# Kernel tuning notes

Hardware: AMD Instinct MI355X
Metric: run time of the kernel (lower is better)

The kernel has to match this reference:

```python
import jax, jax.numpy as jnp
import numpy as np

P = 2        # patch size (all 3 dims)
NB = 8       # num_bands
N = 16       # d_state
DTR = 8      # dt_rank = d_model // 16
DCONV = 4    # d_conv
SMAX = 2.0   # smax_dt = smax_B = smax_C


def _ln(x, g, b):
    mu = x.mean(-1, keepdims=True)
    v = ((x - mu) ** 2).mean(-1, keepdims=True)
    return (x - mu) / jnp.sqrt(v + 1e-5) * g + b


def _silu(x):
    return x * jax.nn.sigmoid(x)


def _ssm_layer(x, band, m, rho, Win, bin_, convw, convb, Wx, Wdt, bdt, Alog, Dp,
               Wout, bout, edt, eB, eC, wr, wm):
    # x: [B, L, d_model] -> bidirectional conditioned selective scan (BiFCSSM)
    Bsz, L, _ = x.shape
    ED = convw.shape[0]
    xz = x @ Win + bin_
    xp, z = xz[..., :ED], xz[..., ED:]
    # depthwise causal conv1d over L
    xpad = jnp.pad(xp, ((0, 0), (DCONV - 1, 0), (0, 0)))
    xc = sum(xpad[:, k:k + L, :] * convw[:, k] for k in range(DCONV)) + convb
    xc = _silu(xc)
    dbl = xc @ Wx                                    # [B,L,DTR+2N]
    dt = jax.nn.softplus(dbl[..., :DTR] @ Wdt + bdt)  # [B,L,ED]
    # band/radius/mask conditioned modulation of delta, B, C
    s_dt = SMAX * jax.nn.sigmoid(edt[band][None] + wr[0] * rho[None] + wm[0] * m)
    s_B = SMAX * jax.nn.sigmoid(eB[band][None] + wr[1] * rho[None] + wm[1] * m)
    s_C = SMAX * jax.nn.sigmoid(eC[band][None] + wr[2] * rho[None] + wm[2] * m)
    dt = dt * s_dt[..., None]
    Bm = dbl[..., DTR:DTR + N] * s_B[..., None]       # [B,L,N]
    Cm = dbl[..., DTR + N:] * s_C[..., None]          # [B,L,N]
    A = -jnp.exp(Alog)                                # [ED,N]
    dA = jnp.exp(dt[..., None] * A)                   # [B,L,ED,N]
    dBu = (dA - 1.0) / A * Bm[:, :, None, :] * xc[..., None]   # exact ZOH
    dA_s = jnp.moveaxis(dA, 1, 0)
    dBu_s = jnp.moveaxis(dBu, 1, 0)
    C_s = jnp.moveaxis(Cm, 1, 0)
    h0 = jnp.zeros((Bsz, ED, N), x.dtype)

    def step(h, inp):
        a, bu, c = inp
        h = a * h + bu
        return h, jnp.einsum('ben,bn->be', h, c)

    _, yf = jax.lax.scan(step, h0, (dA_s, dBu_s, C_s))
    _, yb = jax.lax.scan(step, h0, (dA_s, dBu_s, C_s), reverse=True)
    y = jnp.moveaxis(yf + yb, 0, 1) + Dp * xc
    y = y * _silu(z)
    return y @ Wout + bout


def _fwd(kspace_ri, mask, pe_w, pe_b, pu_w, pu_b, ln_g, ln_b, fn_g, fn_b,
         cond_band, cond_rad_w, cond_mask_w, l0_Win, l0_bin, l0_convw, l0_convb,
         l0_Wx, l0_Wdt, l0_bdt, l0_Alog, l0_D, l0_Wout, l0_bout, l0_edt, l0_eB,
         l0_eC, l0_wr, l0_wm):
    Bsz, C, nx, ny, nz = kspace_ri.shape
    gx, gy, gz = nx // P, ny // P, nz // P
    L = gx * gy * gz
    # patch embed (Conv3d, kernel==stride) as blocked einsum
    xr = kspace_ri.reshape(Bsz, C, gx, P, gy, P, gz, P)
    x = jnp.einsum('bcxiyjzk,dcijk->bdxyz', xr, pe_w) + pe_b[None, :, None, None, None]
    DM = x.shape[1]
    x = x.reshape(Bsz, DM, L).transpose(0, 2, 1)               # [B,L,D]
    m = mask.reshape(Bsz, 1, gx, P, gy, P, gz, P).mean(axis=(3, 5, 7)).reshape(Bsz, L)
    m = jnp.clip(m, 0.0, 1.0)
    # raster scan ordering: identity permutation, rho_bar, band ids
    rho = jnp.arange(L, dtype=x.dtype) / float(L - 1)
    band = jnp.clip(jnp.floor(rho * NB).astype(jnp.int32), 0, NB - 1)
    # condition tokens
    cond = cond_band[band][None] + rho[None, :, None] * cond_rad_w + m[:, :, None] * cond_mask_w
    h = _ln(x + cond, ln_g, ln_b)
    h = h + _ssm_layer(_ln(h, fn_g, fn_b), band, m, rho, l0_Win, l0_bin, l0_convw,
                       l0_convb, l0_Wx, l0_Wdt, l0_bdt, l0_Alog, l0_D, l0_Wout,
                       l0_bout, l0_edt, l0_eB, l0_eC, l0_wr, l0_wm)
    # patch unembed (ConvTranspose3d, kernel==stride) as blocked einsum
    hg = h.transpose(0, 2, 1).reshape(Bsz, DM, gx, gy, gz)
    out = jnp.einsum('bdxyz,dcijk->bcxiyjzk', hg, pu_w).reshape(Bsz, C, nx, ny, nz)
    out = out + pu_b[None, :, None, None, None]
    return kspace_ri + out


def setup_inputs() -> dict:
    key = jax.random.key(0)
    ks = jax.random.split(key, 24)
    ED, DM, CIN = 256, 128, 16

    def nrm(k, shape, s):
        return jax.random.normal(k, shape, jnp.float32) * s

    return {
        'kspace_ri': jax.random.normal(ks[0], (1, CIN, 64, 64, 16), jnp.float32),
        'mask': jax.random.uniform(ks[1], (1, 1, 64, 64, 16), jnp.float32),
        'pe_w': nrm(ks[2], (DM, CIN, P, P, P), 0.09),
        'pe_b': nrm(ks[3], (DM,), 0.02),
        'pu_w': nrm(ks[4], (DM, CIN, P, P, P), 0.05),
        'pu_b': jnp.zeros((CIN,), jnp.float32),
        'ln_g': jnp.ones((DM,), jnp.float32),
        'ln_b': jnp.zeros((DM,), jnp.float32),
        'fn_g': jnp.ones((DM,), jnp.float32),
        'fn_b': jnp.zeros((DM,), jnp.float32),
        'cond_band': nrm(ks[5], (NB, DM), 0.02),
        'cond_rad_w': nrm(ks[6], (DM,), 0.02),
        'cond_mask_w': nrm(ks[7], (DM,), 0.02),
        'l0_Win': nrm(ks[8], (DM, 2 * ED), 0.05),
        'l0_bin': jnp.zeros((2 * ED,), jnp.float32),
        'l0_convw': nrm(ks[9], (ED, DCONV), 0.2),
        'l0_convb': jnp.zeros((ED,), jnp.float32),
        'l0_Wx': nrm(ks[10], (ED, DTR + 2 * N), 0.05),
        'l0_Wdt': nrm(ks[11], (DTR, ED), 0.1),
        'l0_bdt': jnp.full((ED,), -3.0, jnp.float32),
        'l0_Alog': jnp.log(jnp.tile(jnp.arange(1, N + 1, dtype=jnp.float32), (ED, 1))),
        'l0_D': jnp.ones((ED,), jnp.float32),
        'l0_Wout': nrm(ks[12], (ED, DM), 0.05),
        'l0_bout': jnp.zeros((DM,), jnp.float32),
        'l0_edt': nrm(ks[13], (NB,), 0.1),
        'l0_eB': nrm(ks[14], (NB,), 0.1),
        'l0_eC': nrm(ks[15], (NB,), 0.1),
        'l0_wr': nrm(ks[16], (3,), 0.1),
        'l0_wm': nrm(ks[17], (3,), 0.1),
    }


def reference(kspace_ri, mask, pe_w, pe_b, pu_w, pu_b, ln_g, ln_b, fn_g, fn_b,
              cond_band, cond_rad_w, cond_mask_w, l0_Win, l0_bin, l0_convw,
              l0_convb, l0_Wx, l0_Wdt, l0_bdt, l0_Alog, l0_D, l0_Wout, l0_bout,
              l0_edt, l0_eB, l0_eC, l0_wr, l0_wm):
    return _fwd(kspace_ri, mask, pe_w, pe_b, pu_w, pu_b, ln_g, ln_b, fn_g, fn_b,
                cond_band, cond_rad_w, cond_mask_w, l0_Win, l0_bin, l0_convw,
                l0_convb, l0_Wx, l0_Wdt, l0_bdt, l0_Alog, l0_D, l0_Wout, l0_bout,
                l0_edt, l0_eB, l0_eC, l0_wr, l0_wm)
```

## Files before the change

kernel.cpp:

```cpp
#include <hip/hip_runtime.h>
#include <hip/hip_bf16.h>

#define L_TOK 8192
#define NCh 256
#define CLh 32
#define LOG2E 1.44269504088896f

typedef short bf16x8 __attribute__((ext_vector_type(8)));
typedef float f32x4 __attribute__((ext_vector_type(4)));

static __device__ __forceinline__ float nexp2(float x) {
#if __has_builtin(__builtin_amdgcn_exp2f)
    return __builtin_amdgcn_exp2f(x);
#else
    return exp2f(x);
#endif
}
static __device__ __forceinline__ float sigm(float x) {
    return 1.f / (1.f + nexp2(-x * LOG2E));
}
static __device__ __forceinline__ ushort f2bf(float x) {
    union { float f; uint u; } v; v.f = x;
    uint r = v.u + 0x7fffu + ((v.u >> 16) & 1u);
    return (ushort)(r >> 16);
}
static __device__ __forceinline__ float bf2f(ushort h) {
    union { float f; uint u; } v; v.u = ((uint)h) << 16;
    return v.f;
}
static __device__ __forceinline__ void f2hl(float x, ushort* hi, ushort* lo) {
    ushort h = f2bf(x);
    *hi = h;
    *lo = f2bf(x - bf2f(h));
}

#define W_PE   0
#define W_WIN  16384
#define W_WOUT 81920
#define W_PU   114688
#define W_PROJ 131072
#define W_TOT  212992

__global__ __launch_bounds__(256) void prep_k(const float* __restrict__ pe_w, const float* __restrict__ Win,
                                              const float* __restrict__ Wx, const float* __restrict__ Wdt,
                                              const float* __restrict__ Wout, const float* __restrict__ pu_w,
                                              const float* __restrict__ mask,
                                              ushort* __restrict__ wH, ushort* __restrict__ wL,
                                              float* __restrict__ mbuf) {
    int b = blockIdx.x;
    if (b >= 832) {
        int l = (b - 832) * 256 + threadIdx.x;
        int xg = l >> 8, yg = (l >> 3) & 31, zg = l & 7;
        float s = 0.f;
        for (int i2 = 0; i2 < 2; ++i2)
            for (int j2 = 0; j2 < 2; ++j2)
                for (int k2 = 0; k2 < 2; ++k2)
                    s += mask[(2 * xg + i2) * 1024 + (2 * yg + j2) * 16 + 2 * zg + k2];
        s *= 0.125f;
        mbuf[l] = fminf(fmaxf(s, 0.f), 1.f);
        return;
    }
    int i = b * 256 + threadIdx.x;
    float v;
    if (i < 16384) {
        v = pe_w[i];
    } else if (i < 81920) {
        int j = i - 16384; int n = j >> 7, k = j & 127;
        v = Win[k * 512 + n];
    } else if (i < 114688) {
        int j = i - 81920; int n = j >> 8, k = j & 255;
        v = Wout[k * 128 + n];
    } else if (i < 131072) {
        int j = i - 114688; int n = j >> 7, k = j & 127;
        v = pu_w[k * 128 + n];
    } else {
        int j = i - 131072; int n = j >> 8, k = j & 255;
        if (n < 256) {
            float s = 0.f;
#pragma unroll
            for (int r = 0; r < 8; ++r) s += Wx[k * 40 + r] * Wdt[r * 256 + n];
            v = s;
        } else if (n < 288) {
            v = Wx[k * 40 + 8 + (n - 256)];
        } else {
            v = 0.f;
        }
    }
    ushort h, lo; f2hl(v, &h, &lo);
    wH[i] = h; wL[i] = lo;
}

__global__ __launch_bounds__(256) void embed_ln_k(const float* __restrict__ ks,
                                                  const ushort* __restrict__ wH, const ushort* __restrict__ wL,
                                                  const float* __restrict__ pe_b, const float* __restrict__ cond_band,
                                                  const float* __restrict__ cond_rad, const float* __restrict__ cond_mask,
                                                  const float* __restrict__ mbuf,
                                                  const float* __restrict__ ln_g, const float* __restrict__ ln_b,
                                                  const float* __restrict__ fn_g, const float* __restrict__ fn_b,
                                                  float* __restrict__ h_,
                                                  ushort* __restrict__ hnH, ushort* __restrict__ hnL) {
    __shared__ __align__(16) char smem[41472];
    ushort (*AsH)[72] = (ushort(*)[72])(smem);
    ushort (*AsL)[72] = (ushort(*)[72])(smem + 2304);
    ushort (*BsH)[72] = (ushort(*)[72])(smem + 4608);
    ushort (*BsL)[72] = (ushort(*)[72])(smem + 23040);
    float  (*Cs)[132] = (float(*)[132])(smem);

    const int tid = threadIdx.x;
    const int lane = tid & 63, wn = tid >> 6;
    const int ln = lane & 15, q = lane >> 4;
    const int mb = blockIdx.x * 16;

    f32x4 acc[2];
    acc[0] = (f32x4){0.f, 0.f, 0.f, 0.f};
    acc[1] = (f32x4){0.f, 0.f, 0.f, 0.f};

    for (int kc = 0; kc < 128; kc += 64) {
        __syncthreads();
        for (int u = tid; u < 1024; u += 256) {
            int r = u >> 6, kk = u & 63;
            int l = mb + r, k = kc + kk;
            int cc = k >> 3, ijk = k & 7;
            int xg = l >> 8, yg = (l >> 3) & 31, zg = l & 7;
            int i2 = (ijk >> 2) & 1, j2 = (ijk >> 1) & 1, k2 = ijk & 1;
            float v = ks[cc * 65536 + (2 * xg + i2) * 1024 + (2 * yg + j2) * 16 + 2 * zg + k2];
            ushort h, lo; f2hl(v, &h, &lo);
            AsH[r][kk] = h; AsL[r][kk] = lo;
        }
        for (int u = tid; u < 1024; u += 256) {
            int n = u >> 3, g = u & 7;
            *(uint4*)&BsH[n][g * 8] = *(const uint4*)&wH[W_PE + n * 128 + kc + g * 8];
            *(uint4*)&BsL[n][g * 8] = *(const uint4*)&wL[W_PE + n * 128 + kc + g * 8];
        }
        __syncthreads();
#pragma unroll
        for (int ks_ = 0; ks_ < 64; ks_ += 32) {
            const int kk = ks_ + q * 8;
            bf16x8 ah = *(const bf16x8*)&AsH[ln][kk];
            bf16x8 al = *(const bf16x8*)&AsL[ln][kk];
#pragma unroll
            for (int cb = 0; cb < 2; ++cb) {
                bf16x8 bh = *(const bf16x8*)&BsH[wn * 32 + cb * 16 + ln][kk];
                bf16x8 bl = *(const bf16x8*)&BsL[wn * 32 + cb * 16 + ln][kk];
                acc[cb] = __builtin_amdgcn_mfma_f32_16x16x32_bf16(ah, bh, acc[cb], 0, 0, 0);
                acc[cb] = __builtin_amdgcn_mfma_f32_16x16x32_bf16(ah, bl, acc[cb], 0, 0, 0);
                acc[cb] = __builtin_amdgcn_mfma_f32_16x16x32_bf16(al, bh, acc[cb], 0, 0, 0);
            }
        }
    }
    __syncthreads();
#pragma unroll
    for (int cb = 0; cb < 2; ++cb) {
#pragma unroll
        for (int r = 0; r < 4; ++r) {
            int row = q * 4 + r;
            int col = wn * 32 + cb * 16 + ln;
            int l = mb + row;
            float rho = (float)l * (1.0f / 8191.0f);
            int band = min(7, (int)(rho * 8.0f));
            Cs[row][col] = acc[cb][r] + pe_b[col] + cond_band[band * 128 + col]
                           + rho * cond_rad[col] + mbuf[l] * cond_mask[col];
        }
    }
    __syncthreads();
    {
        int row = tid >> 4, j = tid & 15;
        int l = mb + row;
        float v8[8];
        float s = 0.f, s2 = 0.f;
#pragma unroll
        for (int i = 0; i < 8; ++i) {
            float v = Cs[row][j * 8 + i];
            v8[i] = v; s += v; s2 += v * v;
        }
#pragma unroll
        for (int o = 1; o < 16; o <<= 1) { s += __shfl_xor(s, o, 16); s2 += __shfl_xor(s2, o, 16); }
        float mu = s * (1.f / 128.f);
        float var = s2 * (1.f / 128.f) - mu * mu;
        float rstd = rsqrtf(fmaxf(var, 0.f) + 1e-5f);
        float hv[8];
        s = 0.f; s2 = 0.f;
#pragma unroll
        for (int i = 0; i < 8; ++i) {
            int col = j * 8 + i;
            float h = (v8[i] - mu) * rstd * ln_g[col] + ln_b[col];
            hv[i] = h; s += h; s2 += h * h;
        }
#pragma unroll
        for (int i = 0; i < 8; i += 4)
            *(float4*)&h_[(size_t)l * 128 + j * 8 + i] = make_float4(hv[i], hv[i + 1], hv[i + 2], hv[i + 3]);
#pragma unroll
        for (int o = 1; o < 16; o <<= 1) { s += __shfl_xor(s, o, 16); s2 += __shfl_xor(s2, o, 16); }
        mu = s * (1.f / 128.f);
        var = s2 * (1.f / 128.f) - mu * mu;
        rstd = rsqrtf(fmaxf(var, 0.f) + 1e-5f);
        union { ushort u[8]; uint4 v4; } oh, ol;
#pragma unroll
        for (int i = 0; i < 8; ++i) {
            int col = j * 8 + i;
            float o2 = (hv[i] - mu) * rstd * fn_g[col] + fn_b[col];
            ushort hh, ll; f2hl(o2, &hh, &ll);
            oh.u[i] = hh; ol.u[i] = ll;
        }
        *(uint4*)&hnH[(size_t)l * 128 + j * 8] = oh.v4;
        *(uint4*)&hnL[(size_t)l * 128 + j * 8] = ol.v4;
    }
}

__global__ __launch_bounds__(256) void win_k(const ushort* __restrict__ Ah, const ushort* __restrict__ Al,
                                             const ushort* __restrict__ wH, const ushort* __restrict__ wL,
                                             const float* __restrict__ bin_,
                                             float* __restrict__ xp, float* __restrict__ sz) {
    __shared__ ushort AsH[64][72], AsL[64][72];
    __shared__ ushort BsH[64][72], BsL[64][72];
    const int tid = threadIdx.x;
    const int lane = tid & 63, wave = tid >> 6;
    const int wm = wave & 1, wn = wave >> 1;
    const int ln = lane & 15, q = lane >> 4;
    const int mb = blockIdx.x * 64, nb = blockIdx.y * 64;

    f32x4 acc[2][2];
#pragma unroll
    for (int rb = 0; rb < 2; ++rb)
#pragma unroll
        for (int cb = 0; cb < 2; ++cb) acc[rb][cb] = (f32x4){0.f, 0.f, 0.f, 0.f};

    for (int kc = 0; kc < 128; kc += 64) {
        __syncthreads();
        for (int u = tid; u < 512; u += 256) {
            int r = u >> 3, g = u & 7;
            size_t go = (size_t)(mb + r) * 128 + kc + g * 8;
            *(uint4*)&AsH[r][g * 8] = *(const uint4*)&Ah[go];
            *(uint4*)&AsL[r][g * 8] = *(const uint4*)&Al[go];
        }
        for (int u = tid; u < 512; u += 256) {
            int n = u >> 3, g = u & 7;
            size_t go = (size_t)(W_WIN) + (size_t)(nb + n) * 128 + kc + g * 8;
            *(uint4*)&BsH[n][g * 8] = *(const uint4*)&wH[go];
            *(uint4*)&BsL[n][g * 8] = *(const uint4*)&wL[go];
        }
        __syncthreads();
#pragma unroll
        for (int ks_ = 0; ks_ < 64; ks_ += 32) {
            const int kk = ks_ + q * 8;
            bf16x8 ah[2], al[2], bh[2], bl[2];
#pragma unroll
            for (int rb = 0; rb < 2; ++rb) {
                ah[rb] = *(const bf16x8*)&AsH[wm * 32 + rb * 16 + ln][kk];
                al[rb] = *(const bf16x8*)&AsL[wm * 32 + rb * 16 + ln][kk];
            }
#pragma unroll
            for (int cb = 0; cb < 2; ++cb) {
                bh[cb] = *(const bf16x8*)&BsH[wn * 32 + cb * 16 + ln][kk];
                bl[cb] = *(const bf16x8*)&BsL[wn * 32 + cb * 16 + ln][kk];
            }
#pragma unroll
            for (int rb = 0; rb < 2; ++rb)
#pragma unroll
                for (int cb = 0; cb < 2; ++cb) {
                    acc[rb][cb] = __builtin_amdgcn_mfma_f32_16x16x32_bf16(ah[rb], bh[cb], acc[rb][cb], 0, 0, 0);
                    acc[rb][cb] = __builtin_amdgcn_mfma_f32_16x16x32_bf16(ah[rb], bl[cb], acc[rb][cb], 0, 0, 0);
                    acc[rb][cb] = __builtin_amdgcn_mfma_f32_16x16x32_bf16(al[rb], bh[cb], acc[rb][cb], 0, 0, 0);
                }
        }
    }
#pragma unroll
    for (int rb = 0; rb < 2; ++rb)
#pragma unroll
        for (int cb = 0; cb < 2; ++cb)
#pragma unroll
            for (int r = 0; r < 4; ++r) {
                int l = mb + wm * 32 + rb * 16 + q * 4 + r;
                int col = nb + wn * 32 + cb * 16 + ln;
                float v = acc[rb][cb][r] + bin_[col];
                if (col < 256) {
                    xp[(size_t)l * 256 + col] = v;
                } else {
                    sz[(size_t)l * 256 + (col - 256)] = v * sigm(v);
                }
            }
}

__global__ __launch_bounds__(256) void conv_k(const float* __restrict__ xp, const float* __restrict__ convw,
                                              const float* __restrict__ convb, float* __restrict__ xc) {
    int id = blockIdx.x * 256 + threadIdx.x;
    int l = id >> 6, e4 = (id & 63) * 4;
    float4 cw[4];
#pragma unroll
    for (int j = 0; j < 4; ++j) cw[j] = *(const float4*)&convw[(e4 + j) * 4];
    float4 cb = *(const float4*)&convb[e4];
    float o[4] = {cb.x, cb.y, cb.z, cb.w};
#pragma unroll
    for (int k = 0; k < 4; ++k) {
        int lp = l - 3 + k;
        if (lp >= 0) {
            float4 t = *(const float4*)&xp[(size_t)lp * 256 + e4];
            o[0] += t.x * ((const float*)&cw[0])[k];
            o[1] += t.y * ((const float*)&cw[1])[k];
            o[2] += t.z * ((const float*)&cw[2])[k];
            o[3] += t.w * ((const float*)&cw[3])[k];
        }
    }
    float4 r;
    r.x = o[0] * sigm(o[0]);
    r.y = o[1] * sigm(o[1]);
    r.z = o[2] * sigm(o[2]);
    r.w = o[3] * sigm(o[3]);
    *(float4*)&xc[(size_t)l * 256 + e4] = r;
}

__global__ __launch_bounds__(256) void proj_k(const float* __restrict__ xc,
                                              const ushort* __restrict__ wH, const ushort* __restrict__ wL,
                                              const float* __restrict__ bdt, const float* __restrict__ mbuf,
                                              const float* __restrict__ edt, const float* __restrict__ eB,
                                              const float* __restrict__ eC, const float* __restrict__ wr,
                                              const float* __restrict__ wm,
                                              float* __restrict__ dt, float* __restrict__ Bm, float* __restrict__ Cm) {
    __shared__ ushort AsH[64][72], AsL[64][72];
    __shared__ ushort BsH[64][72], BsL[64][72];
    const int tid = threadIdx.x;
    const int lane = tid & 63, wave = tid >> 6;
    const int wm_ = wave & 1, wn = wave >> 1;
    const int ln = lane & 15, q = lane >> 4;
    const int mb = blockIdx.x * 64, nb = blockIdx.y * 64;

    f32x4 acc[2][2];
#pragma unroll
    for (int rb = 0; rb < 2; ++rb)
#pragma unroll
        for (int cb = 0; cb < 2; ++cb) acc[rb][cb] = (f32x4){0.f, 0.f, 0.f, 0.f};

    for (int kc = 0; kc < 256; kc += 64) {
        __syncthreads();
        for (int u = tid; u < 1024; u += 256) {
            int r = u >> 4, kq = u & 15;
            float4 v = *(const float4*)&xc[(size_t)(mb + r) * 256 + kc + kq * 4];
            union { ushort u[4]; uint2 v2; } hh, ll;
            f2hl(v.x, &hh.u[0], &ll.u[0]); f2hl(v.y, &hh.u[1], &ll.u[1]);
            f2hl(v.z, &hh.u[2], &ll.u[2]); f2hl(v.w, &hh.u[3], &ll.u[3]);
            *(uint2*)&AsH[r][kq * 4] = hh.v2;
            *(uint2*)&AsL[r][kq * 4] = ll.v2;
        }
        for (int u = tid; u < 512; u += 256) {
            int n = u >> 3, g = u & 7;
            size_t go = (size_t)(W_PROJ) + (size_t)(nb + n) * 256 + kc + g * 8;
            *(uint4*)&BsH[n][g * 8] = *(const uint4*)&wH[go];
            *(uint4*)&BsL[n][g * 8] = *(const uint4*)&wL[go];
        }
        __syncthreads();
#pragma unroll
        for (int ks_ = 0; ks_ < 64; ks_ += 32) {
            const int kk = ks_ + q * 8;
            bf16x8 ah[2], al[2], bh[2], bl[2];
#pragma unroll
            for (int rb = 0; rb < 2; ++rb) {
                ah[rb] = *(const bf16x8*)&AsH[wm_ * 32 + rb * 16 + ln][kk];
                al[rb] = *(const bf16x8*)&AsL[wm_ * 32 + rb * 16 + ln][kk];
            }
#pragma unroll
            for (int cb = 0; cb < 2; ++cb) {
                bh[cb] = *(const bf16x8*)&BsH[wn * 32 + cb * 16 + ln][kk];
                bl[cb] = *(const bf16x8*)&BsL[wn * 32 + cb * 16 + ln][kk];
            }
#pragma unroll
            for (int rb = 0; rb < 2; ++rb)
#pragma unroll
                for (int cb = 0; cb < 2; ++cb) {
                    acc[rb][cb] = __builtin_amdgcn_mfma_f32_16x16x32_bf16(ah[rb], bh[cb], acc[rb][cb], 0, 0, 0);
                    acc[rb][cb] = __builtin_amdgcn_mfma_f32_16x16x32_bf16(ah[rb], bl[cb], acc[rb][cb], 0, 0, 0);
                    acc[rb][cb] = __builtin_amdgcn_mfma_f32_16x16x32_bf16(al[rb], bh[cb], acc[rb][cb], 0, 0, 0);
                }
        }
    }
#pragma unroll
    for (int rb = 0; rb < 2; ++rb)
#pragma unroll
        for (int cb = 0; cb < 2; ++cb)
#pragma unroll
            for (int r = 0; r < 4; ++r) {
                int l = mb + wm_ * 32 + rb * 16 + q * 4 + r;
                int col = nb + wn * 32 + cb * 16 + ln;
                float v = acc[rb][cb][r];
                float rho = (float)l * (1.0f / 8191.0f);
                int band = min(7, (int)(rho * 8.0f));
                float mv = mbuf[l];
                if (col < 256) {
                    float sc0 = 2.0f * sigm(edt[band] + wr[0] * rho + wm[0] * mv);
                    float v2 = v + bdt[col];
                    float sp = (v2 > 20.f) ? v2 : log1pf(expf(v2));
                    dt[(size_t)l * 256 + col] = sp * sc0;
                } else if (col < 272) {
                    float sc1 = 2.0f * sigm(eB[band] + wr[1] * rho + wm[1] * mv);
                    Bm[(size_t)l * 16 + (col - 256)] = v * sc1;
                } else if (col < 288) {
                    float sc2 = 2.0f * sigm(eC[band] + wr[2] * rho + wm[2] * mv);
                    Cm[(size_t)l * 16 + (col - 272)] = v * sc2;
                }
            }
}

__global__ __launch_bounds__(256) void scan0_k(const float* __restrict__ dt, const float* __restrict__ xc,
                                               const float* __restrict__ Bm, const float* __restrict__ Alog,
                                               float* __restrict__ Hb, float* __restrict__ sdtb) {
    const int c = blockIdx.x, dir = blockIdx.y, e = threadIdx.x;
    __shared__ float bms[CLh][16];
    for (int idx = e; idx < CLh * 16; idx += 256)
        bms[idx >> 4][idx & 15] = Bm[c * (CLh * 16) + idx];
    float A2[16], iv[16], h[16];
#pragma unroll
    for (int n = 0; n < 16; ++n) {
        float ea = nexp2(Alog[e * 16 + n] * LOG2E);
        A2[n] = -ea * LOG2E;
        iv[n] = -1.0f / ea;
        h[n] = 0.f;
    }
    const int base = c * CLh;
    float cu[8], cx[8], nu[8], nx[8];
#pragma unroll
    for (int j = 0; j < 8; ++j) {
        int p = dir ? (CLh - 1 - j) : j;
        cu[j] = dt[(size_t)(base + p) * 256 + e];
        cx[j] = xc[(size_t)(base + p) * 256 + e];
    }
    __syncthreads();
    float sdt = 0.f;
#pragma unroll
    for (int g = 0; g < CLh / 8; ++g) {
        if (g + 1 < CLh / 8) {
#pragma unroll
            for (int j = 0; j < 8; ++j) {
                int s = (g + 1) * 8 + j;
                int p = dir ? (CLh - 1 - s) : s;
                nu[j] = dt[(size_t)(base + p) * 256 + e];
                nx[j] = xc[(size_t)(base + p) * 256 + e];
            }
        }
#pragma unroll
        for (int j = 0; j < 8; ++j) {
            int s = g * 8 + j;
            int p = dir ? (CLh - 1 - s) : s;
            float u = cu[j], xv = cx[j];
            union { float4 v[4]; float f[16]; } bb;
            const float4* bp = (const float4*)&bms[p][0];
            bb.v[0] = bp[0]; bb.v[1] = bp[1]; bb.v[2] = bp[2]; bb.v[3] = bp[3];
#pragma unroll
            for (int n = 0; n < 16; ++n) {
                float a = nexp2(A2[n] * u);
                float w = xv * bb.f[n] * iv[n];
                h[n] = a * (h[n] + w) - w;
            }
            sdt += u;
        }
#pragma unroll
        for (int j = 0; j < 8; ++j) { cu[j] = nu[j]; cx[j] = nx[j]; }
    }
    const size_t hofs = (size_t)(dir * NCh + c) * 4096 + e * 16;
#pragma unroll
    for (int j = 0; j < 4; ++j)
        *(float4*)&Hb[hofs + 4 * j] = make_float4(h[4 * j], h[4 * j + 1], h[4 * j + 2], h[4 * j + 3]);
    if (dir == 0) sdtb[c * 256 + e] = sdt;
}

__global__ __launch_bounds__(64) void combine_k(const float* __restrict__ Hb, float* __restrict__ Hpre,
                                                const float* __restrict__ sdtb, const float* __restrict__ Alog) {
    int id = blockIdx.x * 64 + threadIdx.x;
    int dir = id >> 12, en = id & 4095, e = en >> 4;
    float A2 = -nexp2(Alog[en] * LOG2E) * LOG2E;
    float hi = 0.f;
    for (int g = 0; g < NCh / 8; ++g) {
        float Pv[8], qv[8];
#pragma unroll
        for (int j = 0; j < 8; ++j) {
            int c = dir ? (NCh - 1 - (g * 8 + j)) : (g * 8 + j);
            Pv[j] = sdtb[c * 256 + e];
            qv[j] = Hb[(size_t)(dir * NCh + c) * 4096 + en];
        }
#pragma unroll
        for (int j = 0; j < 8; ++j) {
            int c = dir ? (NCh - 1 - (g * 8 + j)) : (g * 8 + j);
            float P = nexp2(A2 * Pv[j]);
            Hpre[(size_t)(dir * NCh + c) * 4096 + en] = hi;
            hi = P * hi + qv[j];
        }
    }
}

template <int DIR>
static __device__ __forceinline__ void scan_dir(const float* __restrict__ dt, const float* __restrict__ xc,
                                                int base, int e,
                                                const float (*bms)[16], const float (*cms)[16],
                                                const float* A2, const float* iv,
                                                float* h, float* yreg) {
    float cu[8], cx[8], nu[8], nx[8];
#pragma unroll
    for (int j = 0; j < 8; ++j) {
        const int p = DIR ? (CLh - 1 - j) : j;
        cu[j] = dt[(size_t)(base + p) * 256 + e];
        cx[j] = xc[(size_t)(base + p) * 256 + e];
    }
#pragma unroll
    for (int g = 0; g < CLh / 8; ++g) {
        if (g + 1 < CLh / 8) {
#pragma unroll
            for (int j = 0; j < 8; ++j) {
                const int s = (g + 1) * 8 + j;
                const int p = DIR ? (CLh - 1 - s) : s;
                nu[j] = dt[(size_t)(base + p) * 256 + e];
                nx[j] = xc[(size_t)(base + p) * 256 + e];
            }
        }
#pragma unroll
        for (int j = 0; j < 8; ++j) {
            const int s = g * 8 + j;
            const int p = DIR ? (CLh - 1 - s) : s;
            float u = cu[j], xv = cx[j];
            union { float4 v[4]; float f[16]; } bb, cc;
            const float4* bp = (const float4*)&bms[p][0];
            bb.v[0] = bp[0]; bb.v[1] = bp[1]; bb.v[2] = bp[2]; bb.v[3] = bp[3];
            const float4* cp = (const float4*)&cms[p][0];
            cc.v[0] = cp[0]; cc.v[1] = cp[1]; cc.v[2] = cp[2]; cc.v[3] = cp[3];
            float y = 0.f;
#pragma unroll
            for (int n = 0; n < 16; ++n) {
                float a = nexp2(A2[n] * u);
                float w = xv * bb.f[n] * iv[n];
                h[n] = a * (h[n] + w) - w;
                y += h[n] * cc.f[n];
            }
            yreg[p] = y;
        }
#pragma unroll
        for (int j = 0; j < 8; ++j) { cu[j] = nu[j]; cx[j] = nx[j]; }
    }
}

__global__ __launch_bounds__(512) void scan1g_k(const float* __restrict__ dt, const float* __restrict__ xc,
                                                const float* __restrict__ Bm, const float* __restrict__ Cm,
                                                const float* __restrict__ Alog, const float* __restrict__ Hpre,
                                                const float* __restrict__ sz, const float* __restrict__ Dp,
                                                ushort* __restrict__ AHo, ushort* __restrict__ ALo) {
    const int c = blockIdx.x;
    const int tid = threadIdx.x;
    const int dir = tid >> 8;
    const int e = tid & 255;
    __shared__ float bms[CLh][16];
    __shared__ float cms[CLh][16];
    __shared__ float ysum[CLh][256];
    for (int idx = tid; idx < CLh * 16; idx += 512) {
        bms[idx >> 4][idx & 15] = Bm[c * (CLh * 16) + idx];
        cms[idx >> 4][idx & 15] = Cm[c * (CLh * 16) + idx];
    }
    float A2[16], iv[16], h[16];
#pragma unroll
    for (int n = 0; n < 16; ++n) {
        float ea = nexp2(Alog[e * 16 + n] * LOG2E);
        A2[n] = -ea * LOG2E;
        iv[n] = -1.0f / ea;
    }
    const size_t hofs = (size_t)(dir * NCh + c) * 4096 + e * 16;
#pragma unroll
    for (int j = 0; j < 4; ++j) {
        float4 hv = *(const float4*)&Hpre[hofs + 4 * j];
        h[4 * j] = hv.x; h[4 * j + 1] = hv.y; h[4 * j + 2] = hv.z; h[4 * j + 3] = hv.w;
    }
    const int base = c * CLh;
    float yreg[CLh];
    __syncthreads();
    if (dir == 0) {
        scan_dir<0>(dt, xc, base, e, bms, cms, A2, iv, h, yreg);
    } else {
        scan_dir<1>(dt, xc, base, e, bms, cms, A2, iv, h, yreg);
    }
    __syncthreads();
    if (dir == 0) {
#pragma unroll
        for (int l = 0; l < CLh; ++l) ysum[l][e] = yreg[l];
    }
    __syncthreads();
    if (dir == 1) {
        float dpv = Dp[e];
#pragma unroll
        for (int l = 0; l < CLh; ++l) {
            size_t gl = (size_t)(base + l) * 256 + e;
            float a = (ysum[l][e] + yreg[l] + dpv * xc[gl]) * sz[gl];
            ushort hh, ll; f2hl(a, &hh, &ll);
            AHo[gl] = hh; ALo[gl] = ll;
        }
    }
}

__global__ __launch_bounds__(256) void wout_k(const ushort* __restrict__ AH, const ushort* __restrict__ AL,
                                              const ushort* __restrict__ wH, const ushort* __restrict__ wL,
                                              const float* __restrict__ bout, const float* __restrict__ h_,
                                              ushort* __restrict__ hfH, ushort* __restrict__ hfL) {
    __shared__ ushort AsH[32][72], AsL[32][72];
    __shared__ ushort BsH[64][72], BsL[64][72];
    const int tid = threadIdx.x;
    const int lane = tid & 63, wave = tid >> 6;
    const int wm = wave & 1, wn = wave >> 1;
    const int ln = lane & 15, q = lane >> 4;
    const int mb = blockIdx.x * 32, nb = blockIdx.y * 64;

    f32x4 acc[2];
    acc[0] = (f32x4){0.f, 0.f, 0.f, 0.f};
    acc[1] = (f32x4){0.f, 0.f, 0.f, 0.f};

    for (int kc = 0; kc < 256; kc += 64) {
        __syncthreads();
        for (int u = tid; u < 256; u += 256) {
            int r = u >> 3, g = u & 7;
            size_t go = (size_t)(mb + r) * 256 + kc + g * 8;
            *(uint4*)&AsH[r][g * 8] = *(const uint4*)&AH[go];
            *(uint4*)&AsL[r][g * 8] = *(const uint4*)&AL[go];
        }
        for (int u = tid; u < 512; u += 256) {
            int n = u >> 3, g = u & 7;
            size_t go = (size_t)(W_WOUT) + (size_t)(nb + n) * 256 + kc + g * 8;
            *(uint4*)&BsH[n][g * 8] = *(const uint4*)&wH[go];
            *(uint4*)&BsL[n][g * 8] = *(const uint4*)&wL[go];
        }
        __syncthreads();
#pragma unroll
        for (int ks_ = 0; ks_ < 64; ks_ += 32) {
            const int kk = ks_ + q * 8;
            bf16x8 ah = *(const bf16x8*)&AsH[wm * 16 + ln][kk];
            bf16x8 al = *(const bf16x8*)&AsL[wm * 16 + ln][kk];
#pragma unroll
            for (int cb = 0; cb < 2; ++cb) {
                bf16x8 bh = *(const bf16x8*)&BsH[wn * 32 + cb * 16 + ln][kk];
                bf16x8 bl = *(const bf16x8*)&BsL[wn * 32 + cb * 16 + ln][kk];
                acc[cb] = __builtin_amdgcn_mfma_f32_16x16x32_bf16(ah, bh, acc[cb], 0, 0, 0);
                acc[cb] = __builtin_amdgcn_mfma_f32_16x16x32_bf16(ah, bl, acc[cb], 0, 0, 0);
                acc[cb] = __builtin_amdgcn_mfma_f32_16x16x32_bf16(al, bh, acc[cb], 0, 0, 0);
            }
        }
    }
#pragma unroll
    for (int cb = 0; cb < 2; ++cb)
#pragma unroll
        for (int r = 0; r < 4; ++r) {
            int l = mb + wm * 16 + q * 4 + r;
            int col = nb + wn * 32 + cb * 16 + ln;
            float v = acc[cb][r] + bout[col] + h_[(size_t)l * 128 + col];
            ushort hh, ll; f2hl(v, &hh, &ll);
            hfH[(size_t)l * 128 + col] = hh;
            hfL[(size_t)l * 128 + col] = ll;
        }
}

__global__ __launch_bounds__(256) void unembed_k(const ushort* __restrict__ Ah, const ushort* __restrict__ Al,
                                                 const ushort* __restrict__ wH, const ushort* __restrict__ wL,
                                                 const float* __restrict__ pu_b, const float* __restrict__ ks,
                                                 float* __restrict__ out) {
    __shared__ ushort AsH[32][72], AsL[32][72];
    __shared__ ushort BsH[64][72], BsL[64][72];
    const int tid = threadIdx.x;
    const int lane = tid & 63, wave = tid >> 6;
    const int wm = wave & 1, wn = wave >> 1;
    const int ln = lane & 15, q = lane >> 4;
    const int mb = blockIdx.x * 32, nb = blockIdx.y * 64;

    f32x4 acc[2];
    acc[0] = (f32x4){0.f, 0.f, 0.f, 0.f};
    acc[1] = (f32x4){0.f, 0.f, 0.f, 0.f};

    for (int kc = 0; kc < 128; kc += 64) {
        __syncthreads();
        for (int u = tid; u < 256; u += 256) {
            int r = u >> 3, g = u & 7;
            size_t go = (size_t)(mb + r) * 128 + kc + g * 8;
            *(uint4*)&AsH[r][g * 8] = *(const uint4*)&Ah[go];
            *(uint4*)&AsL[r][g * 8] = *(const uint4*)&Al[go];
        }
        for (int u = tid; u < 512; u += 256) {
            int n = u >> 3, g = u & 7;
            size_t go = (size_t)(W_PU) + (size_t)(nb + n) * 128 + kc + g * 8;
            *(uint4*)&BsH[n][g * 8] = *(const uint4*)&wH[go];
            *(uint4*)&BsL[n][g * 8] = *(const uint4*)&wL[go];
        }
        __syncthreads();
#pragma unroll
        for (int ks_ = 0; ks_ < 64; ks_ += 32) {
            const int kk = ks_ + q * 8;
            bf16x8 ah = *(const bf16x8*)&AsH[wm * 16 + ln][kk];
            bf16x8 al = *(const bf16x8*)&AsL[wm * 16 + ln][kk];
#pragma unroll
            for (int cb = 0; cb < 2; ++cb) {
                bf16x8 bh = *(const bf16x8*)&BsH[wn * 32 + cb * 16 + ln][kk];
                bf16x8 bl = *(const bf16x8*)&BsL[wn * 32 + cb * 16 + ln][kk];
                acc[cb] = __builtin_amdgcn_mfma_f32_16x16x32_bf16(ah, bh, acc[cb], 0, 0, 0);
                acc[cb] = __builtin_amdgcn_mfma_f32_16x16x32_bf16(ah, bl, acc[cb], 0, 0, 0);
                acc[cb] = __builtin_amdgcn_mfma_f32_16x16x32_bf16(al, bh, acc[cb], 0, 0, 0);
            }
        }
    }
#pragma unroll
    for (int cb = 0; cb < 2; ++cb)
#pragma unroll
        for (int r = 0; r < 4; ++r) {
            int l = mb + wm * 16 + q * 4 + r;
            int col = nb + wn * 32 + cb * 16 + ln;
            int xg = l >> 8, yg = (l >> 3) & 31, zg = l & 7;
            int c = col >> 3, ijk = col & 7;
            int i2 = (ijk >> 2) & 1, j2 = (ijk >> 1) & 1, k2 = ijk & 1;
            size_t idx = (size_t)((c * 64 + 2 * xg + i2) * 64 + (2 * yg + j2)) * 16 + 2 * zg + k2;
            out[idx] = acc[cb][r] + pu_b[c] + ks[idx];
        }
}

extern "C" void kernel_launch(void* const* d_in, const int* in_sizes, int n_in,
                              void* d_out, int out_size, void* d_ws, size_t ws_size,
                              hipStream_t stream) {
    const float* ks    = (const float*)d_in[0];
    const float* mask  = (const float*)d_in[1];
    const float* pe_w  = (const float*)d_in[2];
    const float* pe_b  = (const float*)d_in[3];
    const float* pu_w  = (const float*)d_in[4];
    const float* pu_b  = (const float*)d_in[5];
    const float* ln_g  = (const float*)d_in[6];
    const float* ln_b  = (const float*)d_in[7];
    const float* fn_g  = (const float*)d_in[8];
    const float* fn_b  = (const float*)d_in[9];
    const float* cond_band = (const float*)d_in[10];
    const float* cond_rad  = (const float*)d_in[11];
    const float* cond_mask = (const float*)d_in[12];
    const float* Win   = (const float*)d_in[13];
    const float* bin_  = (const float*)d_in[14];
    const float* convw = (const float*)d_in[15];
    const float* convb = (const float*)d_in[16];
    const float* Wx    = (const float*)d_in[17];
    const float* Wdt   = (const float*)d_in[18];
    const float* bdt   = (const float*)d_in[19];
    const float* Alog  = (const float*)d_in[20];
    const float* Dp    = (const float*)d_in[21];
    const float* Wout  = (const float*)d_in[22];
    const float* bout  = (const float*)d_in[23];
    const float* edt   = (const float*)d_in[24];
    const float* eB    = (const float*)d_in[25];
    const float* eC    = (const float*)d_in[26];
    const float* wr    = (const float*)d_in[27];
    const float* wm    = (const float*)d_in[28];
    float* out = (float*)d_out;

    char* base = (char*)d_ws;
    size_t o = 0;
    auto alloc = [&](size_t bytes) { char* p = base + o; o += (bytes + 255) & ~(size_t)255; return p; };
    float*  mbuf = (float*)alloc(32768);
    ushort* wH   = (ushort*)alloc(W_TOT * 2);
    ushort* wL   = (ushort*)alloc(W_TOT * 2);
    float*  h_   = (float*)alloc(4194304);
    ushort* hnH  = (ushort*)alloc(2097152);
    ushort* hnL  = (ushort*)alloc(2097152);
    float*  xp   = (float*)alloc(8388608);
    float*  sz   = (float*)alloc(8388608);
    float*  xc   = (float*)alloc(8388608);
    float*  dt   = (float*)alloc(8388608);
    float*  Bm   = (float*)alloc(524288);
    float*  Cm   = (float*)alloc(524288);
    float*  Hb   = (float*)alloc(8388608);
    float*  Hpre = (float*)alloc(8388608);
    float*  sdtb = (float*)alloc(262144);
    ushort* AHo  = (ushort*)alloc(4194304);
    ushort* ALo  = (ushort*)alloc(4194304);
    ushort* hfH  = (ushort*)alloc(2097152);
    ushort* hfL  = (ushort*)alloc(2097152);

    prep_k<<<864, 256, 0, stream>>>(pe_w, Win, Wx, Wdt, Wout, pu_w, mask, wH, wL, mbuf);
    embed_ln_k<<<512, 256, 0, stream>>>(ks, wH, wL, pe_b, cond_band, cond_rad, cond_mask, mbuf,
                                        ln_g, ln_b, fn_g, fn_b, h_, hnH, hnL);
    win_k<<<dim3(128, 8), 256, 0, stream>>>(hnH, hnL, wH, wL, bin_, xp, sz);
    conv_k<<<2048, 256, 0, stream>>>(xp, convw, convb, xc);
    proj_k<<<dim3(128, 5), 256, 0, stream>>>(xc, wH, wL, bdt, mbuf, edt, eB, eC, wr, wm, dt, Bm, Cm);
    scan0_k<<<dim3(NCh, 2), 256, 0, stream>>>(dt, xc, Bm, Alog, Hb, sdtb);
    combine_k<<<128, 64, 0, stream>>>(Hb, Hpre, sdtb, Alog);
    scan1g_k<<<NCh, 512, 0, stream>>>(dt, xc, Bm, Cm, Alog, Hpre, sz, Dp, AHo, ALo);
    wout_k<<<dim3(256, 2), 256, 0, stream>>>(AHo, ALo, wH, wL, bout, h_, hfH, hfL);
    unembed_k<<<dim3(256, 2), 256, 0, stream>>>(hfH, hfL, wH, wL, pu_b, ks, out);
}
```

Baseline: 240.0 us.

## Fuse depthwise conv into x-projection GEMM and stage k-space patches in LDS

The causal depthwise conv plus SiLU now runs inside proj_k. Each 32-row block computes xc for its tokens, writes it to global memory for the scan, and keeps split-bf16 copies in shared memory as the full-K A operand for the projection GEMM. This removes one kernel launch and the extra read of xc. The cost is fewer, larger blocks: the grid drops from 640 to 256 blocks, and each block loops over all five N tiles itself. Separately, embed_ln_k now loads the block's k-space patch region with float4 loads into LDS before the patchify gather, replacing scattered scalar global reads.

```diff
diff --git a/kernel.cpp b/kernel.cpp
--- a/kernel.cpp
+++ b/kernel.cpp
@@ -99,17 +99,27 @@
                                                   const float* __restrict__ fn_g, const float* __restrict__ fn_b,
                                                   float* __restrict__ h_,
                                                   ushort* __restrict__ hnH, ushort* __restrict__ hnL) {
-    __shared__ __align__(16) char smem[41472];
+    __shared__ __align__(16) char smem[50176];
     ushort (*AsH)[72] = (ushort(*)[72])(smem);
     ushort (*AsL)[72] = (ushort(*)[72])(smem + 2304);
     ushort (*BsH)[72] = (ushort(*)[72])(smem + 4608);
     ushort (*BsL)[72] = (ushort(*)[72])(smem + 23040);
+    float*  ksb       = (float*)(smem + 41472);
     float  (*Cs)[132] = (float(*)[132])(smem);
 
     const int tid = threadIdx.x;
     const int lane = tid & 63, wn = tid >> 6;
     const int ln = lane & 15, q = lane >> 4;
     const int mb = blockIdx.x * 16;
+    const int xg = mb >> 8, yg0 = (mb >> 3) & 31;
+
+    for (int v = tid; v < 512; v += 256) {
+        int seg = v >> 2, zq = v & 3;
+        int cc = seg >> 3, i2 = (seg >> 2) & 1, yy = seg & 3;
+        float4 t4 = *(const float4*)&ks[cc * 65536 + (2 * xg + i2) * 1024 + (2 * yg0 + yy) * 16 + zq * 4];
+        int la = seg * 17 + zq * 4;
+        ksb[la] = t4.x; ksb[la + 1] = t4.y; ksb[la + 2] = t4.z; ksb[la + 3] = t4.w;
+    }
 
     f32x4 acc[2];
     acc[0] = (f32x4){0.f, 0.f, 0.f, 0.f};
@@ -119,13 +129,13 @@
         __syncthreads();
         for (int u = tid; u < 1024; u += 256) {
             int r = u >> 6, kk = u & 63;
-            int l = mb + r, k = kc + kk;
+            int k = kc + kk;
             int cc = k >> 3, ijk = k & 7;
-            int xg = l >> 8, yg = (l >> 3) & 31, zg = l & 7;
             int i2 = (ijk >> 2) & 1, j2 = (ijk >> 1) & 1, k2 = ijk & 1;
-            float v = ks[cc * 65536 + (2 * xg + i2) * 1024 + (2 * yg + j2) * 16 + 2 * zg + k2];
-            ushort h, lo; f2hl(v, &h, &lo);
-            AsH[r][kk] = h; AsL[r][kk] = lo;
+            int seg = (cc * 2 + i2) * 4 + (r >> 3) * 2 + j2;
+            float v = ksb[seg * 17 + (r & 7) * 2 + k2];
+            ushort hh, ll; f2hl(v, &hh, &ll);
+            AsH[r][kk] = hh; AsL[r][kk] = ll;
         }
         for (int u = tid; u < 1024; u += 256) {
             int n = u >> 3, g = u & 7;
@@ -281,122 +291,109 @@
             }
 }
 
-__global__ __launch_bounds__(256) void conv_k(const float* __restrict__ xp, const float* __restrict__ convw,
-                                              const float* __restrict__ convb, float* __restrict__ xc) {
-    int id = blockIdx.x * 256 + threadIdx.x;
-    int l = id >> 6, e4 = (id & 63) * 4;
-    float4 cw[4];
-#pragma unroll
-    for (int j = 0; j < 4; ++j) cw[j] = *(const float4*)&convw[(e4 + j) * 4];
-    float4 cb = *(const float4*)&convb[e4];
-    float o[4] = {cb.x, cb.y, cb.z, cb.w};
-#pragma unroll
-    for (int k = 0; k < 4; ++k) {
-        int lp = l - 3 + k;
-        if (lp >= 0) {
-            float4 t = *(const float4*)&xp[(size_t)lp * 256 + e4];
-            o[0] += t.x * ((const float*)&cw[0])[k];
-            o[1] += t.y * ((const float*)&cw[1])[k];
-            o[2] += t.z * ((const float*)&cw[2])[k];
-            o[3] += t.w * ((const float*)&cw[3])[k];
-        }
-    }
-    float4 r;
-    r.x = o[0] * sigm(o[0]);
-    r.y = o[1] * sigm(o[1]);
-    r.z = o[2] * sigm(o[2]);
-    r.w = o[3] * sigm(o[3]);
-    *(float4*)&xc[(size_t)l * 256 + e4] = r;
-}
-
-__global__ __launch_bounds__(256) void proj_k(const float* __restrict__ xc,
+__global__ __launch_bounds__(512) void proj_k(const float* __restrict__ xp,
+                                              const float* __restrict__ convw, const float* __restrict__ convb,
                                               const ushort* __restrict__ wH, const ushort* __restrict__ wL,
                                               const float* __restrict__ bdt, const float* __restrict__ mbuf,
                                               const float* __restrict__ edt, const float* __restrict__ eB,
                                               const float* __restrict__ eC, const float* __restrict__ wr,
                                               const float* __restrict__ wm,
-                                              float* __restrict__ dt, float* __restrict__ Bm, float* __restrict__ Cm) {
-    __shared__ ushort AsH[64][72], AsL[64][72];
-    __shared__ ushort BsH[64][72], BsL[64][72];
+                                              float* __restrict__ xc, float* __restrict__ dt,
+                                              float* __restrict__ Bm, float* __restrict__ Cm) {
+    __shared__ __align__(16) char smem[52224];
+    ushort (*AsH)[264] = (ushort(*)[264])(smem);
+    ushort (*AsL)[264] = (ushort(*)[264])(smem + 16896);
+    ushort (*BsH)[72]  = (ushort(*)[72])(smem + 33792);
+    ushort (*BsL)[72]  = (ushort(*)[72])(smem + 43008);
     const int tid = threadIdx.x;
+    const int mb = blockIdx.x * 32;
+
+    {
+        const int cg = tid & 63;
+        const int rg = tid >> 6;
+        const int c0 = cg * 4;
+        float4 cb4 = *(const float4*)&convb[c0];
+        float4 cw0 = *(const float4*)&convw[(c0 + 0) * 4];
+        float4 cw1 = *(const float4*)&convw[(c0 + 1) * 4];
+        float4 cw2 = *(const float4*)&convw[(c0 + 2) * 4];
+        float4 cw3 = *(const float4*)&convw[(c0 + 3) * 4];
+        const int lbase = mb + rg * 4;
+        float4 zero = make_float4(0.f, 0.f, 0.f, 0.f);
+        float4 x0 = (lbase - 3 >= 0) ? *(const float4*)&xp[(size_t)(lbase - 3) * 256 + c0] : zero;
+        float4 x1 = (lbase - 2 >= 0) ? *(const float4*)&xp[(size_t)(lbase - 2) * 256 + c0] : zero;
+        float4 x2 = (lbase - 1 >= 0) ? *(const float4*)&xp[(size_t)(lbase - 1) * 256 + c0] : zero;
+#pragma unroll
+        for (int rr = 0; rr < 4; ++rr) {
+            int l = lbase + rr;
+            float4 x3 = *(const float4*)&xp[(size_t)l * 256 + c0];
+            float o0 = cb4.x + x0.x * cw0.x + x1.x * cw0.y + x2.x * cw0.z + x3.x * cw0.w;
+            float o1 = cb4.y + x0.y * cw1.x + x1.y * cw1.y + x2.y * cw1.z + x3.y * cw1.w;
+            float o2 = cb4.z + x0.z * cw2.x + x1.z * cw2.y + x2.z * cw2.z + x3.z * cw2.w;
+            float o3 = cb4.w + x0.w * cw3.x + x1.w * cw3.y + x2.w * cw3.z + x3.w * cw3.w;
+            o0 *= sigm(o0); o1 *= sigm(o1); o2 *= sigm(o2); o3 *= sigm(o3);
+            *(float4*)&xc[(size_t)l * 256 + c0] = make_float4(o0, o1, o2, o3);
+            union { ushort u[4]; uint2 v2; } hh, ll;
+            f2hl(o0, &hh.u[0], &ll.u[0]); f2hl(o1, &hh.u[1], &ll.u[1]);
+            f2hl(o2, &hh.u[2], &ll.u[2]); f2hl(o3, &hh.u[3], &ll.u[3]);
+            int row = l - mb;
+            *(uint2*)&AsH[row][c0] = hh.v2;
+            *(uint2*)&AsL[row][c0] = ll.v2;
+            x0 = x1; x1 = x2; x2 = x3;
+        }
+    }
+    __syncthreads();
+
     const int lane = tid & 63, wave = tid >> 6;
-    const int wm_ = wave & 1, wn = wave >> 1;
+    const int wm2 = wave & 1, wn4 = wave >> 1;
     const int ln = lane & 15, q = lane >> 4;
-    const int mb = blockIdx.x * 64, nb = blockIdx.y * 64;
-
-    f32x4 acc[2][2];
-#pragma unroll
-    for (int rb = 0; rb < 2; ++rb)
-#pragma unroll
-        for (int cb = 0; cb < 2; ++cb) acc[rb][cb] = (f32x4){0.f, 0.f, 0.f, 0.f};
-
-    for (int kc = 0; kc < 256; kc += 64) {
-        __syncthreads();
-        for (int u = tid; u < 1024; u += 256) {
-            int r = u >> 4, kq = u & 15;
-            float4 v = *(const float4*)&xc[(size_t)(mb + r) * 256 + kc + kq * 4];
-            union { ushort u[4]; uint2 v2; } hh, ll;
-            f2hl(v.x, &hh.u[0], &ll.u[0]); f2hl(v.y, &hh.u[1], &ll.u[1]);
-            f2hl(v.z, &hh.u[2], &ll.u[2]); f2hl(v.w, &hh.u[3], &ll.u[3]);
-            *(uint2*)&AsH[r][kq * 4] = hh.v2;
-            *(uint2*)&AsL[r][kq * 4] = ll.v2;
-        }
-        for (int u = tid; u < 512; u += 256) {
-            int n = u >> 3, g = u & 7;
-            size_t go = (size_t)(W_PROJ) + (size_t)(nb + n) * 256 + kc + g * 8;
-            *(uint4*)&BsH[n][g * 8] = *(const uint4*)&wH[go];
-            *(uint4*)&BsL[n][g * 8] = *(const uint4*)&wL[go];
-        }
-        __syncthreads();
-#pragma unroll
-        for (int ks_ = 0; ks_ < 64; ks_ += 32) {
-            const int kk = ks_ + q * 8;
-            bf16x8 ah[2], al[2], bh[2], bl[2];
-#pragma unroll
-            for (int rb = 0; rb < 2; ++rb) {
-                ah[rb] = *(const bf16x8*)&AsH[wm_ * 32 + rb * 16 + ln][kk];
-                al[rb] = *(const bf16x8*)&AsL[wm_ * 32 + rb * 16 + ln][kk];
-            }
-#pragma unroll
-            for (int cb = 0; cb < 2; ++cb) {
-                bh[cb] = *(const bf16x8*)&BsH[wn * 32 + cb * 16 + ln][kk];
-                bl[cb] = *(const bf16x8*)&BsL[wn * 32 + cb * 16 + ln][kk];
-            }
-#pragma unroll
-            for (int rb = 0; rb < 2; ++rb)
-#pragma unroll
-                for (int cb = 0; cb < 2; ++cb) {
-                    acc[rb][cb] = __builtin_amdgcn_mfma_f32_16x16x32_bf16(ah[rb], bh[cb], acc[rb][cb], 0, 0, 0);
-                    acc[rb][cb] = __builtin_amdgcn_mfma_f32_16x16x32_bf16(ah[rb], bl[cb], acc[rb][cb], 0, 0, 0);
-                    acc[rb][cb] = __builtin_amdgcn_mfma_f32_16x16x32_bf16(al[rb], bh[cb], acc[rb][cb], 0, 0, 0);
-                }
-        }
-    }
-#pragma unroll
-    for (int rb = 0; rb < 2; ++rb)
-#pragma unroll
-        for (int cb = 0; cb < 2; ++cb)
-#pragma unroll
-            for (int r = 0; r < 4; ++r) {
-                int l = mb + wm_ * 32 + rb * 16 + q * 4 + r;
-                int col = nb + wn * 32 + cb * 16 + ln;
-                float v = acc[rb][cb][r];
-                float rho = (float)l * (1.0f / 8191.0f);
-                int band = min(7, (int)(rho * 8.0f));
-                float mv = mbuf[l];
-                if (col < 256) {
-                    float sc0 = 2.0f * sigm(edt[band] + wr[0] * rho + wm[0] * mv);
-                    float v2 = v + bdt[col];
-                    float sp = (v2 > 20.f) ? v2 : log1pf(expf(v2));
-                    dt[(size_t)l * 256 + col] = sp * sc0;
-                } else if (col < 272) {
-                    float sc1 = 2.0f * sigm(eB[band] + wr[1] * rho + wm[1] * mv);
-                    Bm[(size_t)l * 16 + (col - 256)] = v * sc1;
-                } else if (col < 288) {
-                    float sc2 = 2.0f * sigm(eC[band] + wr[2] * rho + wm[2] * mv);
-                    Cm[(size_t)l * 16 + (col - 272)] = v * sc2;
-                }
-            }
+    for (int it = 0; it < 5; ++it) {
+        int nb = it * 64;
+        f32x4 acc = (f32x4){0.f, 0.f, 0.f, 0.f};
+        for (int kc = 0; kc < 256; kc += 64) {
+            __syncthreads();
+            {
+                int u = tid;
+                int n = u >> 3, g = u & 7;
+                size_t go = (size_t)(W_PROJ) + (size_t)(nb + n) * 256 + kc + g * 8;
+                *(uint4*)&BsH[n][g * 8] = *(const uint4*)&wH[go];
+                *(uint4*)&BsL[n][g * 8] = *(const uint4*)&wL[go];
+            }
+            __syncthreads();
+#pragma unroll
+            for (int ks_ = 0; ks_ < 64; ks_ += 32) {
+                const int kka = kc + ks_ + q * 8;
+                const int kkb = ks_ + q * 8;
+                bf16x8 ah = *(const bf16x8*)&AsH[wm2 * 16 + ln][kka];
+                bf16x8 al = *(const bf16x8*)&AsL[wm2 * 16 + ln][kka];
+                bf16x8 bh = *(const bf16x8*)&BsH[wn4 * 16 + ln][kkb];
+                bf16x8 bl = *(const bf16x8*)&BsL[wn4 * 16 + ln][kkb];
+                acc = __builtin_amdgcn_mfma_f32_16x16x32_bf16(ah, bh, acc, 0, 0, 0);
+                acc = __builtin_amdgcn_mfma_f32_16x16x32_bf16(ah, bl, acc, 0, 0, 0);
+                acc = __builtin_amdgcn_mfma_f32_16x16x32_bf16(al, bh, acc, 0, 0, 0);
+            }
+        }
+#pragma unroll
+        for (int r = 0; r < 4; ++r) {
+            int l = mb + wm2 * 16 + q * 4 + r;
+            int col = nb + wn4 * 16 + ln;
+            float v = acc[r];
+            float rho = (float)l * (1.0f / 8191.0f);
+            int band = min(7, (int)(rho * 8.0f));
+            float mv = mbuf[l];
+            if (col < 256) {
+                float sc0 = 2.0f * sigm(edt[band] + wr[0] * rho + wm[0] * mv);
+                float v2 = v + bdt[col];
+                float sp = (v2 > 20.f) ? v2 : log1pf(expf(v2));
+                dt[(size_t)l * 256 + col] = sp * sc0;
+            } else if (col < 272) {
+                float sc1 = 2.0f * sigm(eB[band] + wr[1] * rho + wm[1] * mv);
+                Bm[(size_t)l * 16 + (col - 256)] = v * sc1;
+            } else if (col < 288) {
+                float sc2 = 2.0f * sigm(eC[band] + wr[2] * rho + wm[2] * mv);
+                Cm[(size_t)l * 16 + (col - 272)] = v * sc2;
+            }
+        }
+    }
 }
 
 __global__ __launch_bounds__(256) void scan0_k(const float* __restrict__ dt, const float* __restrict__ xc,
@@ -769,8 +766,8 @@
     embed_ln_k<<<512, 256, 0, stream>>>(ks, wH, wL, pe_b, cond_band, cond_rad, cond_mask, mbuf,
                                         ln_g, ln_b, fn_g, fn_b, h_, hnH, hnL);
     win_k<<<dim3(128, 8), 256, 0, stream>>>(hnH, hnL, wH, wL, bin_, xp, sz);
-    conv_k<<<2048, 256, 0, stream>>>(xp, convw, convb, xc);
-    proj_k<<<dim3(128, 5), 256, 0, stream>>>(xc, wH, wL, bdt, mbuf, edt, eB, eC, wr, wm, dt, Bm, Cm);
+    proj_k<<<256, 512, 0, stream>>>(xp, convw, convb, wH, wL, bdt, mbuf, edt, eB, eC, wr, wm,
+                                    xc, dt, Bm, Cm);
     scan0_k<<<dim3(NCh, 2), 256, 0, stream>>>(dt, xc, Bm, Alog, Hb, sdtb);
     combine_k<<<128, 64, 0, stream>>>(Hb, Hpre, sdtb, Alog);
     scan1g_k<<<NCh, 512, 0, stream>>>(dt, xc, Bm, Cm, Alog, Hpre, sz, Dp, AHo, ALo);
```

Measured after the change: 237.4 us (median of 2 runs). About the same (-1.1%).
